# Performance work log

Measured on AMD Instinct MI355X. Metric: run time of the kernel, lower is better.

## Reference

```python
import jax, jax.numpy as jnp
import numpy as np

B, L, D = 2, 512, 128

def setup_inputs() -> dict:
    key = jax.random.key(0)
    ks = jax.random.split(key, 5)
    scale = 1.0 / np.sqrt(D)
    return {
        "s": jax.random.normal(ks[0], (B, L, D), dtype=jnp.float32),
        "h": jax.random.normal(ks[1], (B, L, D), dtype=jnp.float32),
        "W": jax.random.normal(ks[2], (D, D), dtype=jnp.float32) * scale,
        "U": jax.random.normal(ks[3], (D, D), dtype=jnp.float32) * scale,
        "v": jax.random.normal(ks[4], (D, 1), dtype=jnp.float32) * scale,
    }

def reference(s, h, W, U, v):
    # s, h: [B, L, D]; W, U: [D, D]; v: [D, 1]
    sW = s @ W                      # [B, L, D]
    hU = h @ U                      # [B, L, D]
    # additive scores: tanh(sW_i + hU_j) . v  -> [B, L, L]
    scores = jnp.einsum("blmd,d->blm", jnp.tanh(sW[:, :, None, :] + hU[:, None, :, :]), v[:, 0])
    attn = jax.nn.softmax(scores, axis=-1)   # softmax over keys (last axis)
    # dropout p=0 is identity; weighted sum over h
    return jnp.einsum("blm,bmd->bld", attn, h)
```

## Files before the change

### kernel.cpp

```cpp
#include <hip/hip_runtime.h>

#define DD 128
#define LL 512
#define BB 2
#define NK (BB * LL)

__global__ __launch_bounds__(256)
void proj_kernel(const float* __restrict__ s, const float* __restrict__ h,
                 const float* __restrict__ W, const float* __restrict__ U,
                 float* __restrict__ Es, float* __restrict__ EhT4) {
    __shared__ float xr[4 * DD];
    int bx = blockIdx.x;
    bool second = bx >= 256;
    const float* X = second ? h : s;
    const float* M = second ? U : W;
    int row0 = (bx & 255) * 4;
    int t = threadIdx.x;
    xr[t]       = 2.0f * X[row0 * DD + t];
    xr[t + 256] = 2.0f * X[row0 * DD + 256 + t];
    __syncthreads();
    int c = t & 127, g = t >> 7;
    const float* x0 = &xr[(2 * g) * DD];
    const float* x1 = &xr[(2 * g + 1) * DD];
    float a0 = 0.f, a1 = 0.f;
#pragma unroll 8
    for (int d = 0; d < DD; ++d) {
        float m = M[d * DD + c];
        a0 = fmaf(x0[d], m, a0);
        a1 = fmaf(x1[d], m, a1);
    }
    float e0 = __expf(a0);
    float e1 = __expf(a1);
    if (!second) {
        Es[(row0 + 2 * g) * DD + c]     = e0;
        Es[(row0 + 2 * g + 1) * DD + c] = e1;
    } else {
        int base = (c >> 2) * (NK * 4) + (c & 3);
        EhT4[base + (row0 + 2 * g) * 4]     = e0;
        EhT4[base + (row0 + 2 * g + 1) * 4] = e1;
    }
}

__global__ __launch_bounds__(512, 2)
void attn_kernel(const float* __restrict__ Es, const float* __restrict__ EhT4,
                 const float* __restrict__ h, const float* __restrict__ v,
                 float* __restrict__ out) {
    __shared__ float4 p4[LL];
    __shared__ float4 wsum4[8];
    __shared__ float red[8][4][DD];

    int bx = blockIdx.x;
    int row0 = bx * 4;
    int b = bx >> 7;
    int t = threadIdx.x;
    int lane = t & 63;
    int w = __builtin_amdgcn_readfirstlane(t >> 6);

    int j = w * 64 + lane;
    int kk = b * LL + j;
    const float4* hp = (const float4*)EhT4 + kk;
    const float* es0 = Es + (size_t)row0 * DD;
    float ac0 = 0.f, ac1 = 0.f, ac2 = 0.f, ac3 = 0.f;
    float cc0 = 0.f, cc1 = 0.f, cc2 = 0.f, cc3 = 0.f;
#pragma unroll 4
    for (int dg = 0; dg < 32; ++dg) {
        float4 E  = hp[(size_t)dg * NK];
        float4 q0 = *(const float4*)(es0 + 0 * DD + dg * 4);
        float4 q1 = *(const float4*)(es0 + 1 * DD + dg * 4);
        float4 q2 = *(const float4*)(es0 + 2 * DD + dg * 4);
        float4 q3 = *(const float4*)(es0 + 3 * DD + dg * 4);
        float4 vv = *(const float4*)(v + dg * 4);
        float vsxy = vv.x + vv.y;
        float vszw = vv.z + vv.w;
#define PAIR(eqx, eqy, Ehx, Ehy, vx, vy, vs, ACC, CCC)                    \
        {                                                                 \
            float Ex = eqx * Ehx;                                         \
            float Ey = eqy * Ehy;                                         \
            float uy = Ey + 1.f;                                          \
            float den = fmaf(Ex, uy, uy);                                 \
            float r = __builtin_amdgcn_rcpf(den);                         \
            float num = fmaf(vx, Ey, vy * Ex);                            \
            ACC = fmaf(num, r, ACC);                                      \
            CCC = fmaf(vs, r, CCC);                                       \
        }
        PAIR(q0.x, q0.y, E.x, E.y, vv.x, vv.y, vsxy, ac0, cc0)
        PAIR(q0.z, q0.w, E.z, E.w, vv.z, vv.w, vszw, ac0, cc0)
        PAIR(q1.x, q1.y, E.x, E.y, vv.x, vv.y, vsxy, ac1, cc1)
        PAIR(q1.z, q1.w, E.z, E.w, vv.z, vv.w, vszw, ac1, cc1)
        PAIR(q2.x, q2.y, E.x, E.y, vv.x, vv.y, vsxy, ac2, cc2)
        PAIR(q2.z, q2.w, E.z, E.w, vv.z, vv.w, vszw, ac2, cc2)
        PAIR(q3.x, q3.y, E.x, E.y, vv.x, vv.y, vsxy, ac3, cc3)
        PAIR(q3.z, q3.w, E.z, E.w, vv.z, vv.w, vszw, ac3, cc3)
#undef PAIR
    }
    float p0 = __expf(-2.f * (ac0 + cc0));
    float p1 = __expf(-2.f * (ac1 + cc1));
    float p2 = __expf(-2.f * (ac2 + cc2));
    float p3 = __expf(-2.f * (ac3 + cc3));
    p4[j] = make_float4(p0, p1, p2, p3);
    float m0 = p0, m1 = p1, m2 = p2, m3 = p3;
#pragma unroll
    for (int o = 1; o < 64; o <<= 1) {
        m0 += __shfl_xor(m0, o);
        m1 += __shfl_xor(m1, o);
        m2 += __shfl_xor(m2, o);
        m3 += __shfl_xor(m3, o);
    }
    if (lane == 0) wsum4[w] = make_float4(m0, m1, m2, m3);
    __syncthreads();

    int half = lane >> 5;
    int d4 = (lane & 31) * 4;
    const float* hb = h + (size_t)b * LL * DD;
    float4 A0 = make_float4(0.f, 0.f, 0.f, 0.f), A1 = A0, A2 = A0, A3 = A0;
#pragma unroll 4
    for (int jj = 0; jj < 32; ++jj) {
        int jl = w * 64 + jj * 2 + half;
        float4 hv = *(const float4*)&hb[jl * DD + d4];
        float4 pp = p4[jl];
        A0.x = fmaf(pp.x, hv.x, A0.x); A0.y = fmaf(pp.x, hv.y, A0.y);
        A0.z = fmaf(pp.x, hv.z, A0.z); A0.w = fmaf(pp.x, hv.w, A0.w);
        A1.x = fmaf(pp.y, hv.x, A1.x); A1.y = fmaf(pp.y, hv.y, A1.y);
        A1.z = fmaf(pp.y, hv.z, A1.z); A1.w = fmaf(pp.y, hv.w, A1.w);
        A2.x = fmaf(pp.z, hv.x, A2.x); A2.y = fmaf(pp.z, hv.y, A2.y);
        A2.z = fmaf(pp.z, hv.z, A2.z); A2.w = fmaf(pp.z, hv.w, A2.w);
        A3.x = fmaf(pp.w, hv.x, A3.x); A3.y = fmaf(pp.w, hv.y, A3.y);
        A3.z = fmaf(pp.w, hv.z, A3.z); A3.w = fmaf(pp.w, hv.w, A3.w);
    }
#define FOLD(A) A.x += __shfl_xor(A.x, 32); A.y += __shfl_xor(A.y, 32); \
                A.z += __shfl_xor(A.z, 32); A.w += __shfl_xor(A.w, 32);
    FOLD(A0) FOLD(A1) FOLD(A2) FOLD(A3)
#undef FOLD
    if (half == 0) {
        *(float4*)&red[w][0][d4] = A0;
        *(float4*)&red[w][1][d4] = A1;
        *(float4*)&red[w][2][d4] = A2;
        *(float4*)&red[w][3][d4] = A3;
    }
    __syncthreads();

    {
        int q = t >> 7, d = t & 127;
        float o = 0.f;
#pragma unroll
        for (int k = 0; k < 8; ++k) o += red[k][q][d];
        const float* wf = (const float*)wsum4;
        float qs = 0.f;
#pragma unroll
        for (int k = 0; k < 8; ++k) qs += wf[k * 4 + q];
        out[(size_t)(row0 + q) * DD + d] = o * __builtin_amdgcn_rcpf(qs);
    }
}

extern "C" void kernel_launch(void* const* d_in, const int* in_sizes, int n_in,
                              void* d_out, int out_size, void* d_ws, size_t ws_size,
                              hipStream_t stream) {
    const float* s = (const float*)d_in[0];
    const float* h = (const float*)d_in[1];
    const float* W = (const float*)d_in[2];
    const float* U = (const float*)d_in[3];
    const float* v = (const float*)d_in[4];
    float* out = (float*)d_out;
    float* ws  = (float*)d_ws;

    float* Es   = ws;
    float* EhT4 = ws + 131072;

    hipLaunchKernelGGL(proj_kernel, dim3(512), dim3(256), 0, stream,
                       s, h, W, U, Es, EhT4);
    hipLaunchKernelGGL(attn_kernel, dim3(NK / 4), dim3(512), 0, stream,
                       Es, EhT4, h, v, out);
}
```

Measured before the change: 81.61 us.

## Vectorize projection with float4 rows and use packed v2f math in score loop

The projection kernel now handles 8 rows per block, and each thread computes 4 output columns using float4 loads of the weight matrix and float4 stores. This halves the grid and widens memory accesses. The attention score inner loop is rewritten with 2-wide vector types so the compiler can emit packed FP32 ops (v_pk_mul/v_pk_fma), with the numerator and the correction term accumulated together in one packed FMA. The packed form computes the denominator as (Ex+1)(Ey+1) explicitly, which may change the instruction count and rounding slightly.

```diff
diff --git a/kernel.cpp b/kernel.cpp
--- a/kernel.cpp
+++ b/kernel.cpp
@@ -5,39 +5,45 @@
 #define BB 2
 #define NK (BB * LL)
 
+typedef float v2f __attribute__((ext_vector_type(2)));
+
 __global__ __launch_bounds__(256)
 void proj_kernel(const float* __restrict__ s, const float* __restrict__ h,
                  const float* __restrict__ W, const float* __restrict__ U,
                  float* __restrict__ Es, float* __restrict__ EhT4) {
-    __shared__ float xr[4 * DD];
+    __shared__ float xr[8 * DD];
     int bx = blockIdx.x;
-    bool second = bx >= 256;
+    bool second = bx >= 128;
     const float* X = second ? h : s;
     const float* M = second ? U : W;
-    int row0 = (bx & 255) * 4;
+    int row0 = (bx & 127) * 8;
     int t = threadIdx.x;
-    xr[t]       = 2.0f * X[row0 * DD + t];
-    xr[t + 256] = 2.0f * X[row0 * DD + 256 + t];
+    {
+        float4 xv = *(const float4*)&X[row0 * DD + t * 4];
+        xv.x *= 2.f; xv.y *= 2.f; xv.z *= 2.f; xv.w *= 2.f;
+        *(float4*)&xr[t * 4] = xv;
+    }
     __syncthreads();
-    int c = t & 127, g = t >> 7;
-    const float* x0 = &xr[(2 * g) * DD];
-    const float* x1 = &xr[(2 * g + 1) * DD];
-    float a0 = 0.f, a1 = 0.f;
+    int r = t >> 5, cg = (t & 31) * 4;
+    const float* xrow = &xr[r * DD];
+    float4 acc = make_float4(0.f, 0.f, 0.f, 0.f);
 #pragma unroll 8
     for (int d = 0; d < DD; ++d) {
-        float m = M[d * DD + c];
-        a0 = fmaf(x0[d], m, a0);
-        a1 = fmaf(x1[d], m, a1);
+        float4 m = *(const float4*)&M[d * DD + cg];
+        float xb = xrow[d];
+        acc.x = fmaf(xb, m.x, acc.x);
+        acc.y = fmaf(xb, m.y, acc.y);
+        acc.z = fmaf(xb, m.z, acc.z);
+        acc.w = fmaf(xb, m.w, acc.w);
     }
-    float e0 = __expf(a0);
-    float e1 = __expf(a1);
+    float4 e;
+    e.x = __expf(acc.x); e.y = __expf(acc.y);
+    e.z = __expf(acc.z); e.w = __expf(acc.w);
+    int row = row0 + r;
     if (!second) {
-        Es[(row0 + 2 * g) * DD + c]     = e0;
-        Es[(row0 + 2 * g + 1) * DD + c] = e1;
+        *(float4*)&Es[row * DD + cg] = e;
     } else {
-        int base = (c >> 2) * (NK * 4) + (c & 3);
-        EhT4[base + (row0 + 2 * g) * 4]     = e0;
-        EhT4[base + (row0 + 2 * g + 1) * 4] = e1;
+        *(float4*)&EhT4[((size_t)(cg >> 2) * NK + row) * 4] = e;
     }
 }
 
@@ -60,8 +66,7 @@
     int kk = b * LL + j;
     const float4* hp = (const float4*)EhT4 + kk;
     const float* es0 = Es + (size_t)row0 * DD;
-    float ac0 = 0.f, ac1 = 0.f, ac2 = 0.f, ac3 = 0.f;
-    float cc0 = 0.f, cc1 = 0.f, cc2 = 0.f, cc3 = 0.f;
+    v2f ac0 = {0.f, 0.f}, ac1 = {0.f, 0.f}, ac2 = {0.f, 0.f}, ac3 = {0.f, 0.f};
 #pragma unroll 4
     for (int dg = 0; dg < 32; ++dg) {
         float4 E  = hp[(size_t)dg * NK];
@@ -70,33 +75,37 @@
         float4 q2 = *(const float4*)(es0 + 2 * DD + dg * 4);
         float4 q3 = *(const float4*)(es0 + 3 * DD + dg * 4);
         float4 vv = *(const float4*)(v + dg * 4);
+        v2f Exy = {E.x, E.y},   Ezw = {E.z, E.w};
+        v2f vxy = {vv.x, vv.y}, vzw = {vv.z, vv.w};
         float vsxy = vv.x + vv.y;
         float vszw = vv.z + vv.w;
-#define PAIR(eqx, eqy, Ehx, Ehy, vx, vy, vs, ACC, CCC)                    \
+#define PAIRV(es2, Eh2, vv2, vs, ACC)                                     \
         {                                                                 \
-            float Ex = eqx * Ehx;                                         \
-            float Ey = eqy * Ehy;                                         \
-            float uy = Ey + 1.f;                                          \
-            float den = fmaf(Ex, uy, uy);                                 \
-            float r = __builtin_amdgcn_rcpf(den);                         \
-            float num = fmaf(vx, Ey, vy * Ex);                            \
-            ACC = fmaf(num, r, ACC);                                      \
-            CCC = fmaf(vs, r, CCC);                                       \
+            v2f E2 = (es2) * (Eh2);                     \
+            v2f d2 = E2 + 1.0f;                         \
+            float den = d2.x * d2.y;                                      \
+            v2f Esw = __builtin_shufflevector(E2, E2, 1, 0);              \
+            v2f n2 = (vv2) * Esw;                      \
+            float num = n2.x + n2.y;                                      \
+            float rc = __builtin_amdgcn_rcpf(den);                        \
+            v2f nv = {num, vs};                                           \
+            v2f rr = {rc, rc};                                            \
+            ACC = __builtin_elementwise_fma(nv, rr, ACC);     \
         }
-        PAIR(q0.x, q0.y, E.x, E.y, vv.x, vv.y, vsxy, ac0, cc0)
-        PAIR(q0.z, q0.w, E.z, E.w, vv.z, vv.w, vszw, ac0, cc0)
-        PAIR(q1.x, q1.y, E.x, E.y, vv.x, vv.y, vsxy, ac1, cc1)
-        PAIR(q1.z, q1.w, E.z, E.w, vv.z, vv.w, vszw, ac1, cc1)
-        PAIR(q2.x, q2.y, E.x, E.y, vv.x, vv.y, vsxy, ac2, cc2)
-        PAIR(q2.z, q2.w, E.z, E.w, vv.z, vv.w, vszw, ac2, cc2)
-        PAIR(q3.x, q3.y, E.x, E.y, vv.x, vv.y, vsxy, ac3, cc3)
-        PAIR(q3.z, q3.w, E.z, E.w, vv.z, vv.w, vszw, ac3, cc3)
-#undef PAIR
+        PAIRV(((v2f){q0.x, q0.y}), Exy, vxy, vsxy, ac0)
+        PAIRV(((v2f){q0.z, q0.w}), Ezw, vzw, vszw, ac0)
+        PAIRV(((v2f){q1.x, q1.y}), Exy, vxy, vsxy, ac1)
+        PAIRV(((v2f){q1.z, q1.w}), Ezw, vzw, vszw, ac1)
+        PAIRV(((v2f){q2.x, q2.y}), Exy, vxy, vsxy, ac2)
+        PAIRV(((v2f){q2.z, q2.w}), Ezw, vzw, vszw, ac2)
+        PAIRV(((v2f){q3.x, q3.y}), Exy, vxy, vsxy, ac3)
+        PAIRV(((v2f){q3.z, q3.w}), Ezw, vzw, vszw, ac3)
+#undef PAIRV
     }
-    float p0 = __expf(-2.f * (ac0 + cc0));
-    float p1 = __expf(-2.f * (ac1 + cc1));
-    float p2 = __expf(-2.f * (ac2 + cc2));
-    float p3 = __expf(-2.f * (ac3 + cc3));
+    float p0 = __expf(-2.f * (ac0.x + ac0.y));
+    float p1 = __expf(-2.f * (ac1.x + ac1.y));
+    float p2 = __expf(-2.f * (ac2.x + ac2.y));
+    float p3 = __expf(-2.f * (ac3.x + ac3.y));
     p4[j] = make_float4(p0, p1, p2, p3);
     float m0 = p0, m1 = p1, m2 = p2, m3 = p3;
 #pragma unroll
@@ -166,7 +175,7 @@
     float* Es   = ws;
     float* EhT4 = ws + 131072;
 
-    hipLaunchKernelGGL(proj_kernel, dim3(512), dim3(256), 0, stream,
+    hipLaunchKernelGGL(proj_kernel, dim3(256), dim3(256), 0, stream,
                        s, h, W, U, Es, EhT4);
     hipLaunchKernelGGL(attn_kernel, dim3(NK / 4), dim3(512), 0, stream,
                        Es, EhT4, h, v, out);
```

After: 84.59 us. +3.7%, slower.

## Fuse projection and attention kernels into one cooperative launch with grid sync

Applied to the files above, without the earlier changes.

Merges the separate projection kernel into the attention kernel. Each block now projects its own 4 query rows and 4 key rows (exp of 2*x@W and 2*x@U), writes them to workspace, and then waits on a grid-wide barrier before the attention phase. The aim is to remove the second kernel launch and its launch gap. In exchange it adds a cooperative grid sync, uses only half the threads for the projection phase, and lowers the launch-bounds occupancy hint from 2 to 1.

```diff
diff --git a/kernel.cpp b/kernel.cpp
--- a/kernel.cpp
+++ b/kernel.cpp
@@ -1,50 +1,20 @@
 #include <hip/hip_runtime.h>
+#include <hip/hip_cooperative_groups.h>
+
+namespace cg = cooperative_groups;
 
 #define DD 128
 #define LL 512
 #define BB 2
 #define NK (BB * LL)
 
-__global__ __launch_bounds__(256)
-void proj_kernel(const float* __restrict__ s, const float* __restrict__ h,
-                 const float* __restrict__ W, const float* __restrict__ U,
-                 float* __restrict__ Es, float* __restrict__ EhT4) {
-    __shared__ float xr[4 * DD];
-    int bx = blockIdx.x;
-    bool second = bx >= 256;
-    const float* X = second ? h : s;
-    const float* M = second ? U : W;
-    int row0 = (bx & 255) * 4;
-    int t = threadIdx.x;
-    xr[t]       = 2.0f * X[row0 * DD + t];
-    xr[t + 256] = 2.0f * X[row0 * DD + 256 + t];
-    __syncthreads();
-    int c = t & 127, g = t >> 7;
-    const float* x0 = &xr[(2 * g) * DD];
-    const float* x1 = &xr[(2 * g + 1) * DD];
-    float a0 = 0.f, a1 = 0.f;
-#pragma unroll 8
-    for (int d = 0; d < DD; ++d) {
-        float m = M[d * DD + c];
-        a0 = fmaf(x0[d], m, a0);
-        a1 = fmaf(x1[d], m, a1);
-    }
-    float e0 = __expf(a0);
-    float e1 = __expf(a1);
-    if (!second) {
-        Es[(row0 + 2 * g) * DD + c]     = e0;
-        Es[(row0 + 2 * g + 1) * DD + c] = e1;
-    } else {
-        int base = (c >> 2) * (NK * 4) + (c & 3);
-        EhT4[base + (row0 + 2 * g) * 4]     = e0;
-        EhT4[base + (row0 + 2 * g + 1) * 4] = e1;
-    }
-}
-
-__global__ __launch_bounds__(512, 2)
-void attn_kernel(const float* __restrict__ Es, const float* __restrict__ EhT4,
-                 const float* __restrict__ h, const float* __restrict__ v,
-                 float* __restrict__ out) {
+__global__ __launch_bounds__(512, 1)
+void fused_kernel(const float* __restrict__ s, const float* __restrict__ h,
+                  const float* __restrict__ W, const float* __restrict__ U,
+                  const float* __restrict__ v,
+                  float* __restrict__ Es, float* __restrict__ EhT4,
+                  float* __restrict__ out) {
+    __shared__ float xr[8 * DD];
     __shared__ float4 p4[LL];
     __shared__ float4 wsum4[8];
     __shared__ float red[8][4][DD];
@@ -55,6 +25,45 @@
     int t = threadIdx.x;
     int lane = t & 63;
     int w = __builtin_amdgcn_readfirstlane(t >> 6);
+
+    {
+        int e2 = t * 2;
+        int row8 = e2 >> 7;
+        int col = e2 & 127;
+        const float* src = (row8 < 4) ? s : h;
+        int grow = row0 + (row8 & 3);
+        float2 xv = *(const float2*)&src[(size_t)grow * DD + col];
+        xr[row8 * DD + col]     = 2.f * xv.x;
+        xr[row8 * DD + col + 1] = 2.f * xv.y;
+    }
+    __syncthreads();
+    if (t < 256) {
+        int half = t >> 7;
+        int r = (t >> 5) & 3;
+        int cg4 = (t & 31) * 4;
+        const float* M = half ? U : W;
+        const float* xrow = &xr[(half * 4 + r) * DD];
+        float4 acc = make_float4(0.f, 0.f, 0.f, 0.f);
+#pragma unroll 8
+        for (int d = 0; d < DD; ++d) {
+            float4 m = *(const float4*)&M[d * DD + cg4];
+            float xb = xrow[d];
+            acc.x = fmaf(xb, m.x, acc.x);
+            acc.y = fmaf(xb, m.y, acc.y);
+            acc.z = fmaf(xb, m.z, acc.z);
+            acc.w = fmaf(xb, m.w, acc.w);
+        }
+        float4 e;
+        e.x = __expf(acc.x); e.y = __expf(acc.y);
+        e.z = __expf(acc.z); e.w = __expf(acc.w);
+        int row = row0 + r;
+        if (half == 0) {
+            *(float4*)&Es[(size_t)row * DD + cg4] = e;
+        } else {
+            *(float4*)&EhT4[((size_t)(cg4 >> 2) * NK + row) * 4] = e;
+        }
+    }
+    cg::this_grid().sync();
 
     int j = w * 64 + lane;
     int kk = b * LL + j;
@@ -166,8 +175,8 @@
     float* Es   = ws;
     float* EhT4 = ws + 131072;
 
-    hipLaunchKernelGGL(proj_kernel, dim3(512), dim3(256), 0, stream,
-                       s, h, W, U, Es, EhT4);
-    hipLaunchKernelGGL(attn_kernel, dim3(NK / 4), dim3(512), 0, stream,
-                       Es, EhT4, h, v, out);
+    void* args[] = {(void*)&s, (void*)&h, (void*)&W, (void*)&U, (void*)&v,
+                    (void*)&Es, (void*)&EhT4, (void*)&out};
+    hipLaunchCooperativeKernel((void*)fused_kernel, dim3(NK / 4), dim3(512),
+                               args, 0, stream);
 }
```

Measured after the change: 131.5 us. 1.61x slower.
